# Optimization experiments

Hardware: AMD Instinct MI355X
Metric: run time of the kernel (lower is better)

Reference implementation:

```python
import jax, jax.numpy as jnp
import numpy as np

N_DIM = 2048
M_SEQ = 8192


def setup_inputs() -> dict:
    key = jax.random.key(0)
    k1, k2, k3 = jax.random.split(key, 3)
    scale = 1.0 / np.sqrt(N_DIM)
    x = jax.random.normal(k1, (M_SEQ, N_DIM), dtype=jnp.float32)
    Wx = jax.random.normal(k2, (N_DIM, 3 * N_DIM), dtype=jnp.float32) * scale
    Wh = jax.random.normal(k3, (N_DIM, 3 * N_DIM), dtype=jnp.float32) * scale
    b = jnp.zeros((3 * N_DIM,), dtype=jnp.float32)
    return {"x": x, "Wx": Wx, "Wh": Wh, "b": b}


def _gru_scan(x, Wx, Wh, b):
    n = x.shape[-1]
    # Precompute input projections for all steps in one GEMM: [m_seq, 3n]
    gx = x @ Wx + b

    def step(h, gx_t):
        gh = h @ Wh  # [3n]
        xz, xr, xn = gx_t[:n], gx_t[n:2 * n], gx_t[2 * n:]
        hz, hr, hn = gh[:n], gh[n:2 * n], gh[2 * n:]
        z = jax.nn.sigmoid(xz + hz)
        r = jax.nn.sigmoid(xr + hr)
        cand = jnp.tanh(xn + r * hn)
        h_new = (1.0 - z) * h + z * cand
        return h_new, h_new

    h0 = jnp.zeros((n,), dtype=x.dtype)
    _, out = jax.lax.scan(step, h0, gx)
    return out  # [m_seq, n_dim]


def reference(x, Wx, Wh, b):
    return _gru_scan(x, Wx, Wh, b)
```

## Files before the change

kernel.cpp:

```cpp
#include <hip/hip_runtime.h>
#include <stdint.h>

#define M_SEQ 8192
#define N_DIM 2048
#define N3    (3 * N_DIM)

typedef short bf16x8 __attribute__((ext_vector_type(8)));
typedef float f32x4  __attribute__((ext_vector_type(4)));
typedef unsigned short u16;
typedef unsigned long long u64;

__device__ __forceinline__ u16 f2bf(float f) {
    unsigned int u = __builtin_bit_cast(unsigned int, f);
    u = (u + 0x7fffu + ((u >> 16) & 1u)) >> 16;
    return (u16)u;
}
__device__ __forceinline__ float bf2f(u16 v) {
    return __builtin_bit_cast(float, (unsigned int)v << 16);
}

__global__ void k_tr_bf16(const float* __restrict__ in, u16* __restrict__ out, int R, int C) {
    __shared__ float tile[32][33];
    const int tx = threadIdx.x & 31, ty = threadIdx.x >> 5;
    const int c = blockIdx.x * 32 + tx;
#pragma unroll
    for (int k = 0; k < 4; ++k)
        tile[ty + k * 8][tx] = in[(size_t)(blockIdx.y * 32 + ty + k * 8) * C + c];
    __syncthreads();
#pragma unroll
    for (int k = 0; k < 4; ++k)
        out[(size_t)(blockIdx.x * 32 + ty + k * 8) * R + blockIdx.y * 32 + tx] =
            f2bf(tile[tx][ty + k * 8]);
}

__global__ void k_tr_f32(const float* __restrict__ in, float* __restrict__ out, int R, int C) {
    __shared__ float tile[32][33];
    const int tx = threadIdx.x & 31, ty = threadIdx.x >> 5;
    const int c = blockIdx.x * 32 + tx;
#pragma unroll
    for (int k = 0; k < 4; ++k)
        tile[ty + k * 8][tx] = in[(size_t)(blockIdx.y * 32 + ty + k * 8) * C + c];
    __syncthreads();
#pragma unroll
    for (int k = 0; k < 4; ++k)
        out[(size_t)(blockIdx.x * 32 + ty + k * 8) * R + blockIdx.y * 32 + tx] =
            tile[tx][ty + k * 8];
}

__global__ void k_init(u64* hbuf) {
    int i = blockIdx.x * 256 + threadIdx.x;
    if (i < N_DIM) hbuf[i] = 0ull;
}

template <typename GXT>
__global__ __launch_bounds__(256) void k_gemm(const float* __restrict__ A,
                                              const u16* __restrict__ B,
                                              const float* __restrict__ bias,
                                              GXT* __restrict__ C) {
    __shared__ u16 As[128 * 32];
    __shared__ u16 Bs[128 * 32];
    const int tid = threadIdx.x, lane = tid & 63, wave = tid >> 6;
    const int m0 = blockIdx.y * 128, n0 = blockIdx.x * 128;
    const int wm = (wave >> 1) * 64, wn = (wave & 1) * 64;
    const int row0 = tid >> 2, ko0 = (tid & 3) * 8;

    f32x4 acc[4][4] = {};

    for (int k0 = 0; k0 < N_DIM; k0 += 32) {
        const float* ap0 = A + (size_t)(m0 + row0) * N_DIM + k0 + ko0;
        const float* ap1 = A + (size_t)(m0 + 64 + row0) * N_DIM + k0 + ko0;
        float4 a0l = *(const float4*)(ap0), a0h = *(const float4*)(ap0 + 4);
        float4 a1l = *(const float4*)(ap1), a1h = *(const float4*)(ap1 + 4);
        bf16x8 a0, a1;
        a0[0] = (short)f2bf(a0l.x); a0[1] = (short)f2bf(a0l.y);
        a0[2] = (short)f2bf(a0l.z); a0[3] = (short)f2bf(a0l.w);
        a0[4] = (short)f2bf(a0h.x); a0[5] = (short)f2bf(a0h.y);
        a0[6] = (short)f2bf(a0h.z); a0[7] = (short)f2bf(a0h.w);
        a1[0] = (short)f2bf(a1l.x); a1[1] = (short)f2bf(a1l.y);
        a1[2] = (short)f2bf(a1l.z); a1[3] = (short)f2bf(a1l.w);
        a1[4] = (short)f2bf(a1h.x); a1[5] = (short)f2bf(a1h.y);
        a1[6] = (short)f2bf(a1h.z); a1[7] = (short)f2bf(a1h.w);
        bf16x8 b0 = *(const bf16x8*)(B + (size_t)(n0 + row0) * N_DIM + k0 + ko0);
        bf16x8 b1 = *(const bf16x8*)(B + (size_t)(n0 + 64 + row0) * N_DIM + k0 + ko0);
        __syncthreads();
        *(bf16x8*)(As + row0 * 32 + ko0)        = a0;
        *(bf16x8*)(As + (64 + row0) * 32 + ko0) = a1;
        *(bf16x8*)(Bs + row0 * 32 + ko0)        = b0;
        *(bf16x8*)(Bs + (64 + row0) * 32 + ko0) = b1;
        __syncthreads();

        bf16x8 af[4], bfr[4];
#pragma unroll
        for (int mt = 0; mt < 4; ++mt)
            af[mt] = *(const bf16x8*)(As + (wm + mt * 16 + (lane & 15)) * 32 + (lane >> 4) * 8);
#pragma unroll
        for (int nt = 0; nt < 4; ++nt)
            bfr[nt] = *(const bf16x8*)(Bs + (wn + nt * 16 + (lane & 15)) * 32 + (lane >> 4) * 8);
#pragma unroll
        for (int mt = 0; mt < 4; ++mt)
#pragma unroll
            for (int nt = 0; nt < 4; ++nt)
                acc[mt][nt] = __builtin_amdgcn_mfma_f32_16x16x32_bf16(af[mt], bfr[nt],
                                                                      acc[mt][nt], 0, 0, 0);
    }

#pragma unroll
    for (int mt = 0; mt < 4; ++mt)
#pragma unroll
        for (int nt = 0; nt < 4; ++nt) {
            const int col = n0 + wn + nt * 16 + (lane & 15);
            const float bv = bias[col];
#pragma unroll
            for (int r = 0; r < 4; ++r) {
                const int rowm = m0 + wm + mt * 16 + (lane >> 4) * 4 + r;
                const float v = acc[mt][nt][r] + bv;
                if constexpr (sizeof(GXT) == 2)
                    ((u16*)C)[(size_t)rowm * N3 + col] = f2bf(v);
                else
                    ((float*)C)[(size_t)rowm * N3 + col] = v;
            }
        }
}

template <typename GXT>
__global__ __launch_bounds__(256, 1) void k_scan(const GXT* __restrict__ gx,
                                                 const float* __restrict__ wht,
                                                 float* __restrict__ out,
                                                 u64* __restrict__ hbuf) {
    extern __shared__ float smem[];
    float* h_lds = smem;
    float* red   = smem + N_DIM;

    const int tid = threadIdx.x, lane = tid & 63, wave = tid >> 6;
    const int g = blockIdx.x;

    float wreg[6][32];
#pragma unroll
    for (int c = 0; c < 6; ++c) {
        const int rr = wave * 6 + c;
        const int col = (rr >> 3) * N_DIM + g * 8 + (rr & 7);
        const float* wp = wht + (size_t)col * N_DIM + lane * 8;
#pragma unroll
        for (int q = 0; q < 4; ++q) {
            f32x4 v0 = *(const f32x4*)(wp + q * 512);
            f32x4 v1 = *(const f32x4*)(wp + q * 512 + 4);
#pragma unroll
            for (int j = 0; j < 4; ++j) {
                wreg[c][q * 8 + j]     = v0[j];
                wreg[c][q * 8 + 4 + j] = v1[j];
            }
        }
    }

    for (int t = 0; t < M_SEQ; ++t) {
        u64* cur = hbuf + (size_t)(t & 1) * N_DIM;
        u64* nxt = hbuf + (size_t)((t + 1) & 1) * N_DIM;
        const unsigned int expect = (unsigned int)t;

        float xz = 0.f, xr = 0.f, xn = 0.f;
        if (tid < 8) {
            const GXT* gp = gx + (size_t)t * N3 + g * 8 + tid;
            if constexpr (sizeof(GXT) == 2) {
                xz = bf2f(((const u16*)gp)[0]);
                xr = bf2f(((const u16*)gp)[N_DIM]);
                xn = bf2f(((const u16*)gp)[2 * N_DIM]);
            } else {
                xz = ((const float*)gp)[0];
                xr = ((const float*)gp)[N_DIM];
                xn = ((const float*)gp)[2 * N_DIM];
            }
        }

        {
            u64 v[8];
            for (;;) {
#pragma unroll
                for (int i = 0; i < 8; ++i)
                    v[i] = __hip_atomic_load(cur + tid + i * 256, __ATOMIC_RELAXED,
                                             __HIP_MEMORY_SCOPE_AGENT);
                bool ok = true;
#pragma unroll
                for (int i = 0; i < 8; ++i) ok &= ((unsigned int)(v[i] >> 32) == expect);
                if (ok) break;
                __builtin_amdgcn_s_sleep(1);
            }
#pragma unroll
            for (int i = 0; i < 8; ++i)
                h_lds[tid + i * 256] =
                    __builtin_bit_cast(float, (unsigned int)(v[i] & 0xffffffffu));
        }
        __syncthreads();

        float acc[6] = {};
#pragma unroll
        for (int q = 0; q < 4; ++q) {
            const float* hp = h_lds + q * 512 + lane * 8;
            f32x4 h0 = *(const f32x4*)(hp);
            f32x4 h1 = *(const f32x4*)(hp + 4);
#pragma unroll
            for (int c = 0; c < 6; ++c) {
#pragma unroll
                for (int j = 0; j < 4; ++j) {
                    acc[c] += wreg[c][q * 8 + j]     * h0[j];
                    acc[c] += wreg[c][q * 8 + 4 + j] * h1[j];
                }
            }
        }
#pragma unroll
        for (int c = 0; c < 6; ++c) {
            float a = acc[c];
#pragma unroll
            for (int off = 32; off; off >>= 1) a += __shfl_xor(a, off, 64);
            if (lane == 0) red[wave * 6 + c] = a;
        }
        __syncthreads();

        if (tid < 8) {
            const float hz = red[tid], hr = red[8 + tid], hn = red[16 + tid];
            const float h_old = h_lds[g * 8 + tid];
            const float z = 1.f / (1.f + __expf(-(xz + hz)));
            const float r = 1.f / (1.f + __expf(-(xr + hr)));
            const float a2 = xn + r * hn;
            const float cand = 1.f - 2.f / (__expf(2.f * a2) + 1.f);
            const float hnew = (1.f - z) * h_old + z * cand;
            out[(size_t)t * N_DIM + g * 8 + tid] = hnew;
            const u64 slot = ((u64)(unsigned int)(t + 1) << 32) |
                             (u64)__builtin_bit_cast(unsigned int, hnew);
            __hip_atomic_store(nxt + g * 8 + tid, slot, __ATOMIC_RELAXED,
                               __HIP_MEMORY_SCOPE_AGENT);
        }
        __syncthreads();
    }
}

extern "C" void kernel_launch(void* const* d_in, const int* in_sizes, int n_in,
                              void* d_out, int out_size, void* d_ws, size_t ws_size,
                              hipStream_t stream) {
    const float* x  = (const float*)d_in[0];
    const float* Wx = (const float*)d_in[1];
    const float* Wh = (const float*)d_in[2];
    const float* b  = (const float*)d_in[3];
    float* out = (float*)d_out;

    char* ws = (char*)d_ws;
    size_t off = 0;
    auto alloc = [&](size_t bytes) -> char* {
        char* p = ws + off;
        off += (bytes + 255) & ~(size_t)255;
        return p;
    };

    u16*   wxt  = (u16*)  alloc((size_t)N3 * N_DIM * sizeof(u16));
    float* wht  = (float*)alloc((size_t)N3 * N_DIM * sizeof(float));
    u64*   hbuf = (u64*)  alloc((size_t)2 * N_DIM * sizeof(u64));

    const bool gx_f32 = ws_size >= (size_t)290 * 1024 * 1024;

    k_init<<<8, 256, 0, stream>>>(hbuf);
    k_tr_bf16<<<dim3(N3 / 32, N_DIM / 32), 256, 0, stream>>>(Wx, wxt, N_DIM, N3);
    k_tr_f32 <<<dim3(N3 / 32, N_DIM / 32), 256, 0, stream>>>(Wh, wht, N_DIM, N3);

    const unsigned smem = (N_DIM + 32) * sizeof(float);
    if (gx_f32) {
        float* gx = (float*)alloc((size_t)M_SEQ * N3 * sizeof(float));
        k_gemm<float><<<dim3(N3 / 128, M_SEQ / 128), 256, 0, stream>>>(x, wxt, b, gx);
        void* args[] = {(void*)&gx, (void*)&wht, (void*)&out, (void*)&hbuf};
        hipError_t e = hipLaunchCooperativeKernel((const void*)k_scan<float>, dim3(256),
                                                  dim3(256), args, smem, stream);
        if (e != hipSuccess)
            k_scan<float><<<256, 256, smem, stream>>>(gx, wht, out, hbuf);
    } else {
        u16* gx = (u16*)alloc((size_t)M_SEQ * N3 * sizeof(u16));
        k_gemm<u16><<<dim3(N3 / 128, M_SEQ / 128), 256, 0, stream>>>(x, wxt, b, gx);
        void* args[] = {(void*)&gx, (void*)&wht, (void*)&out, (void*)&hbuf};
        hipError_t e = hipLaunchCooperativeKernel((const void*)k_scan<u16>, dim3(256),
                                                  dim3(256), args, smem, stream);
        if (e != hipSuccess)
            k_scan<u16><<<256, 256, smem, stream>>>(gx, wht, out, hbuf);
    }
}
```

Measured before the change: 29.16 ms.

## Compute recurrent matvec directly from polled registers and add adaptive poll backoff

The scan kernel now gives each thread 8 contiguous hidden elements across all 24 output rows, so the polled h values feed the dot products straight from registers. This removes the LDS staging of h and one barrier per step, at the cost of a 4-way cross-wave reduction in the gate thread. The h buffer is stored permuted (tid*256+g) so each thread's loads match its weight slice. An adaptive timer using s_memrealtime sleeps for most of the estimated step period before polling, to cut atomic polling traffic on the shared buffer. The timing heuristic could add latency if the period estimate runs ahead of the real arrival time.

```diff
diff --git a/kernel.cpp b/kernel.cpp
--- a/kernel.cpp
+++ b/kernel.cpp
@@ -127,35 +127,28 @@
                                                  const float* __restrict__ wht,
                                                  float* __restrict__ out,
                                                  u64* __restrict__ hbuf) {
-    extern __shared__ float smem[];
-    float* h_lds = smem;
-    float* red   = smem + N_DIM;
-
+    __shared__ float red[96];
     const int tid = threadIdx.x, lane = tid & 63, wave = tid >> 6;
     const int g = blockIdx.x;
 
-    float wreg[6][32];
-#pragma unroll
-    for (int c = 0; c < 6; ++c) {
-        const int rr = wave * 6 + c;
-        const int col = (rr >> 3) * N_DIM + g * 8 + (rr & 7);
-        const float* wp = wht + (size_t)col * N_DIM + lane * 8;
-#pragma unroll
-        for (int q = 0; q < 4; ++q) {
-            f32x4 v0 = *(const f32x4*)(wp + q * 512);
-            f32x4 v1 = *(const f32x4*)(wp + q * 512 + 4);
-#pragma unroll
-            for (int j = 0; j < 4; ++j) {
-                wreg[c][q * 8 + j]     = v0[j];
-                wreg[c][q * 8 + 4 + j] = v1[j];
-            }
-        }
-    }
+    float wreg[24][8];
+#pragma unroll
+    for (int r = 0; r < 24; ++r) {
+        const size_t Cb = ((size_t)((r >> 3) * N_DIM + g * 8 + (r & 7))) * N_DIM + tid * 8;
+        f32x4 w0 = *(const f32x4*)(wht + Cb);
+        f32x4 w1 = *(const f32x4*)(wht + Cb + 4);
+#pragma unroll
+        for (int j = 0; j < 4; ++j) { wreg[r][j] = w0[j]; wreg[r][4 + j] = w1[j]; }
+    }
+
+    float hprev = 0.f;
+    u64 t_last = __builtin_amdgcn_s_memrealtime();
+    unsigned period = 0;
 
     for (int t = 0; t < M_SEQ; ++t) {
         u64* cur = hbuf + (size_t)(t & 1) * N_DIM;
         u64* nxt = hbuf + (size_t)((t + 1) & 1) * N_DIM;
-        const unsigned int expect = (unsigned int)t;
+        const unsigned expect = (unsigned)t;
 
         float xz = 0.f, xr = 0.f, xn = 0.f;
         if (tid < 8) {
@@ -171,62 +164,65 @@
             }
         }
 
+        if (period) {
+            const u64 target = t_last + period - (period >> 2);
+            while ((long long)(target - __builtin_amdgcn_s_memrealtime()) > 0)
+                __builtin_amdgcn_s_sleep(2);
+        }
+
+        u64 v[8];
+        for (;;) {
+#pragma unroll
+            for (int i = 0; i < 8; ++i)
+                v[i] = __hip_atomic_load(cur + tid + (i << 8), __ATOMIC_RELAXED,
+                                         __HIP_MEMORY_SCOPE_AGENT);
+            bool ok = true;
+#pragma unroll
+            for (int i = 0; i < 8; ++i) ok &= ((unsigned)(v[i] >> 32) == expect);
+            if (ok) break;
+            __builtin_amdgcn_s_sleep(1);
+        }
         {
-            u64 v[8];
-            for (;;) {
-#pragma unroll
-                for (int i = 0; i < 8; ++i)
-                    v[i] = __hip_atomic_load(cur + tid + i * 256, __ATOMIC_RELAXED,
-                                             __HIP_MEMORY_SCOPE_AGENT);
-                bool ok = true;
-#pragma unroll
-                for (int i = 0; i < 8; ++i) ok &= ((unsigned int)(v[i] >> 32) == expect);
-                if (ok) break;
-                __builtin_amdgcn_s_sleep(1);
-            }
-#pragma unroll
-            for (int i = 0; i < 8; ++i)
-                h_lds[tid + i * 256] =
-                    __builtin_bit_cast(float, (unsigned int)(v[i] & 0xffffffffu));
-        }
-        __syncthreads();
-
-        float acc[6] = {};
-#pragma unroll
-        for (int q = 0; q < 4; ++q) {
-            const float* hp = h_lds + q * 512 + lane * 8;
-            f32x4 h0 = *(const f32x4*)(hp);
-            f32x4 h1 = *(const f32x4*)(hp + 4);
-#pragma unroll
-            for (int c = 0; c < 6; ++c) {
-#pragma unroll
-                for (int j = 0; j < 4; ++j) {
-                    acc[c] += wreg[c][q * 8 + j]     * h0[j];
-                    acc[c] += wreg[c][q * 8 + 4 + j] * h1[j];
-                }
-            }
-        }
-#pragma unroll
-        for (int c = 0; c < 6; ++c) {
-            float a = acc[c];
+            const u64 now = __builtin_amdgcn_s_memrealtime();
+            const unsigned delta = (unsigned)(now - t_last);
+            t_last = now;
+            if (delta < 8192u)
+                period = period - (period >> 3) + (delta >> 3);
+        }
+
+        float acc[24];
+#pragma unroll
+        for (int r = 0; r < 24; ++r) acc[r] = 0.f;
+#pragma unroll
+        for (int i = 0; i < 8; ++i) {
+            const float hv = __builtin_bit_cast(float, (unsigned)(v[i] & 0xffffffffu));
+#pragma unroll
+            for (int r = 0; r < 24; ++r) acc[r] += wreg[r][i] * hv;
+        }
+
+#pragma unroll
+        for (int r = 0; r < 24; ++r) {
+            float a = acc[r];
 #pragma unroll
             for (int off = 32; off; off >>= 1) a += __shfl_xor(a, off, 64);
-            if (lane == 0) red[wave * 6 + c] = a;
+            if (lane == 0) red[wave * 24 + r] = a;
         }
         __syncthreads();
 
         if (tid < 8) {
-            const float hz = red[tid], hr = red[8 + tid], hn = red[16 + tid];
-            const float h_old = h_lds[g * 8 + tid];
+            const float hz = red[tid]      + red[24 + tid] + red[48 + tid] + red[72 + tid];
+            const float hr = red[8 + tid]  + red[32 + tid] + red[56 + tid] + red[80 + tid];
+            const float hn = red[16 + tid] + red[40 + tid] + red[64 + tid] + red[88 + tid];
             const float z = 1.f / (1.f + __expf(-(xz + hz)));
             const float r = 1.f / (1.f + __expf(-(xr + hr)));
             const float a2 = xn + r * hn;
             const float cand = 1.f - 2.f / (__expf(2.f * a2) + 1.f);
-            const float hnew = (1.f - z) * h_old + z * cand;
+            const float hnew = (1.f - z) * hprev + z * cand;
+            hprev = hnew;
             out[(size_t)t * N_DIM + g * 8 + tid] = hnew;
-            const u64 slot = ((u64)(unsigned int)(t + 1) << 32) |
-                             (u64)__builtin_bit_cast(unsigned int, hnew);
-            __hip_atomic_store(nxt + g * 8 + tid, slot, __ATOMIC_RELAXED,
+            const u64 slot = ((u64)(unsigned)(t + 1) << 32) |
+                             (u64)__builtin_bit_cast(unsigned, hnew);
+            __hip_atomic_store(nxt + tid * 256 + g, slot, __ATOMIC_RELAXED,
                                __HIP_MEMORY_SCOPE_AGENT);
         }
         __syncthreads();
@@ -260,22 +256,21 @@
     k_tr_bf16<<<dim3(N3 / 32, N_DIM / 32), 256, 0, stream>>>(Wx, wxt, N_DIM, N3);
     k_tr_f32 <<<dim3(N3 / 32, N_DIM / 32), 256, 0, stream>>>(Wh, wht, N_DIM, N3);
 
-    const unsigned smem = (N_DIM + 32) * sizeof(float);
     if (gx_f32) {
         float* gx = (float*)alloc((size_t)M_SEQ * N3 * sizeof(float));
         k_gemm<float><<<dim3(N3 / 128, M_SEQ / 128), 256, 0, stream>>>(x, wxt, b, gx);
         void* args[] = {(void*)&gx, (void*)&wht, (void*)&out, (void*)&hbuf};
         hipError_t e = hipLaunchCooperativeKernel((const void*)k_scan<float>, dim3(256),
-                                                  dim3(256), args, smem, stream);
+                                                  dim3(256), args, 0, stream);
         if (e != hipSuccess)
-            k_scan<float><<<256, 256, smem, stream>>>(gx, wht, out, hbuf);
+            k_scan<float><<<256, 256, 0, stream>>>(gx, wht, out, hbuf);
     } else {
         u16* gx = (u16*)alloc((size_t)M_SEQ * N3 * sizeof(u16));
         k_gemm<u16><<<dim3(N3 / 128, M_SEQ / 128), 256, 0, stream>>>(x, wxt, b, gx);
         void* args[] = {(void*)&gx, (void*)&wht, (void*)&out, (void*)&hbuf};
         hipError_t e = hipLaunchCooperativeKernel((const void*)k_scan<u16>, dim3(256),
-                                                  dim3(256), args, smem, stream);
+                                                  dim3(256), args, 0, stream);
         if (e != hipSuccess)
-            k_scan<u16><<<256, 256, smem, stream>>>(gx, wht, out, hbuf);
-    }
-}
+            k_scan<u16><<<256, 256, 0, stream>>>(gx, wht, out, hbuf);
+    }
+}
```

Result: slower. 64.76 ms (+122.1%).
